# Performance work log

Hardware: AMD Instinct MI355X
Metric: run time of the kernel (lower is better)

Reference implementation:

```python
import jax, jax.numpy as jnp
import numpy as np

TEMPERATURE = 0.1
NEG_INF = -1e9
EPS = 1e-12

def setup_inputs() -> dict:
    key = jax.random.key(0)
    k1, k2, k3 = jax.random.split(key, 3)
    B, C, H, W = 8, 256, 128, 128
    num_classes = 150
    features = jax.random.normal(k1, (B, C, H, W), dtype=jnp.float32)
    labels = jax.random.randint(k2, (B, H, W), 0, num_classes, dtype=jnp.int32)
    text_embeddings = jax.random.normal(k3, (num_classes, C), dtype=jnp.float32)
    return {"features": features, "labels": labels, "text_embeddings": text_embeddings, "ignore_index": 255}

def _l2_normalize(x, axis=-1):
    n = jnp.linalg.norm(x, axis=axis, keepdims=True)
    return x / jnp.maximum(n, EPS)

def reference(features, labels, text_embeddings, ignore_index):
    num_classes, C = text_embeddings.shape
    B = features.shape[0]
    # [B,C,H,W] -> [B*H*W, C]
    f = jnp.transpose(features, (0, 2, 3, 1)).reshape(-1, C)
    lab = jnp.where(labels == ignore_index, 0, labels).reshape(-1)
    # segment-mean per class (fused scatter-add instead of per-class loop)
    sums = jax.ops.segment_sum(f, lab, num_segments=num_classes)          # [K,C]
    counts = jax.ops.segment_sum(jnp.ones_like(lab, dtype=f.dtype), lab, num_segments=num_classes)  # [K]
    valid = counts > 0
    prototypes = jnp.where(valid[:, None], sums / jnp.maximum(counts, 1.0)[:, None], 0.0)
    prototypes = _l2_normalize(prototypes)
    text_n = _l2_normalize(text_embeddings)
    sim = (prototypes @ text_n.T) / TEMPERATURE                            # [K,K]
    # cross-entropy restricted to valid rows/cols with identity soft targets
    masked = jnp.where(valid[None, :], sim, NEG_INF)                       # mask invalid cols
    logp = jax.nn.log_softmax(masked, axis=-1)
    diag = jnp.diagonal(logp)
    per_row = jnp.where(valid, -diag, 0.0)
    n_valid = jnp.sum(valid.astype(f.dtype))
    loss = jnp.sum(per_row) / jnp.maximum(n_valid, 1.0)
    return jnp.where(n_valid > 1, loss, 0.0)
```

## Files before the change

kernel.cpp:

```cpp
#include <hip/hip_runtime.h>
#include <math.h>

#define EPSV 1e-12f

typedef __attribute__((ext_vector_type(8))) short short8;
typedef __attribute__((ext_vector_type(4))) float f32x4;

constexpr int MT    = 10;
constexpr int K_PAD = MT * 16;
constexpr int CPB   = 64;
constexpr int CHUNK = 128;
constexpr int PBPX  = 2048;
constexpr int NCHK  = PBPX / CHUNK;
constexpr int NPB   = 64;
constexpr int THR   = 512;
constexpr int LROW  = 136;

__device__ __forceinline__ unsigned short f2bf(float f) {
    unsigned u = __builtin_bit_cast(unsigned, f);
    return (unsigned short)((u + 0x7FFFu + ((u >> 16) & 1u)) >> 16);
}

__global__ __launch_bounds__(THR) void protomm_kernel(
    const float* __restrict__ feat,
    const int*   __restrict__ labels,
    const int*   __restrict__ ign_p,
    float*       __restrict__ partial,
    int C, int HW)
{
    __shared__ unsigned short Bf[CPB * LROW];
    __shared__ int   labL[CHUNK];
    __shared__ float fscr[4][K_PAD * 16];

    const int tid   = threadIdx.x;
    const int w     = tid >> 6;
    const int l     = tid & 63;
    const int ct    = w & 3;
    const int kh    = w >> 2;
    const int rowid = l & 15;
    const int g     = l >> 4;

    const int bid = blockIdx.x;
    const int cg  = bid & 3;
    const int pb  = bid >> 2;
    const int b   = pb >> 3;
    const int px0 = (pb & 7) * PBPX;
    const int ig  = *ign_p;

    const int q   = tid & 31;
    const int chp = tid >> 5;
    const float* fb = feat + ((size_t)(b * C + cg * CPB + chp)) * HW + px0 + 4 * q;
    const int*   lb = labels + (size_t)b * HW + px0;

    f32x4 acc[MT];
    #pragma unroll
    for (int m = 0; m < MT; ++m) acc[m] = (f32x4){0.f, 0.f, 0.f, 0.f};

    float4 pf0, pf1, pf2, pf3;
    int4   plab;
    auto issue = [&](int ck) {
        const float* p = fb + ck * CHUNK;
        pf0 = *reinterpret_cast<const float4*>(p);
        pf1 = *reinterpret_cast<const float4*>(p + (size_t)16 * HW);
        pf2 = *reinterpret_cast<const float4*>(p + (size_t)32 * HW);
        pf3 = *reinterpret_cast<const float4*>(p + (size_t)48 * HW);
        if (tid < 32)
            plab = *reinterpret_cast<const int4*>(lb + ck * CHUNK + 4 * tid);
    };

    issue(0);

    for (int ck = 0; ck < NCHK; ++ck) {
        __syncthreads();
        {
            float4 v[4] = {pf0, pf1, pf2, pf3};
            #pragma unroll
            for (int i = 0; i < 4; ++i) {
                unsigned* dst = reinterpret_cast<unsigned*>(
                    &Bf[(chp + 16 * i) * LROW + 4 * q]);
                dst[0] = (unsigned)f2bf(v[i].x) | ((unsigned)f2bf(v[i].y) << 16);
                dst[1] = (unsigned)f2bf(v[i].z) | ((unsigned)f2bf(v[i].w) << 16);
            }
            if (tid < 32) {
                int4 lv = plab;
                lv.x = (lv.x == ig) ? 0 : lv.x;
                lv.y = (lv.y == ig) ? 0 : lv.y;
                lv.z = (lv.z == ig) ? 0 : lv.z;
                lv.w = (lv.w == ig) ? 0 : lv.w;
                *reinterpret_cast<int4*>(&labL[4 * tid]) = lv;
            }
        }
        __syncthreads();
        if (ck + 1 < NCHK) issue(ck + 1);

        #pragma unroll
        for (int kk = 0; kk < 2; ++kk) {
            const int ks = 2 * kh + kk;
            const int* lp = &labL[ks * 32 + g * 8];
            const int la0 = lp[0], la1 = lp[1], la2 = lp[2], la3 = lp[3];
            const int la4 = lp[4], la5 = lp[5], la6 = lp[6], la7 = lp[7];
            const short8 bfrag = *reinterpret_cast<const short8*>(
                &Bf[(ct * 16 + rowid) * LROW + ks * 32 + g * 8]);
            #pragma unroll
            for (int m = 0; m < MT; ++m) {
                const int tgt = m * 16 + rowid;
                unsigned w0 = (la0 == tgt ? 0x3F80u : 0u) | (la1 == tgt ? 0x3F800000u : 0u);
                unsigned w1 = (la2 == tgt ? 0x3F80u : 0u) | (la3 == tgt ? 0x3F800000u : 0u);
                unsigned w2 = (la4 == tgt ? 0x3F80u : 0u) | (la5 == tgt ? 0x3F800000u : 0u);
                unsigned w3 = (la6 == tgt ? 0x3F80u : 0u) | (la7 == tgt ? 0x3F800000u : 0u);
                uint4 aw = make_uint4(w0, w1, w2, w3);
                short8 afrag = __builtin_bit_cast(short8, aw);
                acc[m] = __builtin_amdgcn_mfma_f32_16x16x32_bf16(afrag, bfrag, acc[m], 0, 0, 0);
            }
        }
    }

    __syncthreads();
    if (kh == 1) {
        #pragma unroll
        for (int m = 0; m < MT; ++m)
            #pragma unroll
            for (int r = 0; r < 4; ++r)
                fscr[ct][(m * 16 + g * 4 + r) * 16 + rowid] = acc[m][r];
    }
    __syncthreads();
    if (kh == 0) {
        float* dst = partial + (size_t)pb * K_PAD * C + cg * CPB + ct * 16 + rowid;
        #pragma unroll
        for (int m = 0; m < MT; ++m)
            #pragma unroll
            for (int r = 0; r < 4; ++r) {
                const int cls = m * 16 + g * 4 + r;
                dst[(size_t)cls * C] = acc[m][r] + fscr[ct][cls * 16 + rowid];
            }
    }
}

__global__ __launch_bounds__(256) void counts_kernel(
    const int* __restrict__ labels, const int* __restrict__ ign_p,
    unsigned int* __restrict__ counts, int N, int K)
{
    __shared__ unsigned int cbins[160];
    const int tid = threadIdx.x;
    for (int i = tid; i < 160; i += 256) cbins[i] = 0u;
    __syncthreads();
    const int ig = *ign_p;
    const int4* l4 = reinterpret_cast<const int4*>(labels);
    const int n4 = N / 4;
    for (int i = blockIdx.x * 256 + tid; i < n4; i += gridDim.x * 256) {
        int4 v = l4[i];
        int a0 = (v.x == ig) ? 0 : v.x;
        int a1 = (v.y == ig) ? 0 : v.y;
        int a2 = (v.z == ig) ? 0 : v.z;
        int a3 = (v.w == ig) ? 0 : v.w;
        if ((unsigned)a0 < (unsigned)K) atomicAdd(&cbins[a0], 1u);
        if ((unsigned)a1 < (unsigned)K) atomicAdd(&cbins[a1], 1u);
        if ((unsigned)a2 < (unsigned)K) atomicAdd(&cbins[a2], 1u);
        if ((unsigned)a3 < (unsigned)K) atomicAdd(&cbins[a3], 1u);
    }
    __syncthreads();
    for (int i = tid; i < K; i += 256)
        if (cbins[i]) atomicAdd(&counts[i], cbins[i]);
}

__global__ __launch_bounds__(256) void normprep_kernel(
    const float* __restrict__ partial,
    const unsigned int* __restrict__ counts,
    const float* __restrict__ text,
    float* __restrict__ proto_n,
    float* __restrict__ text_n,
    float* __restrict__ vmask,
    int K, int C)
{
    const int bid  = blockIdx.x;
    const int tid  = threadIdx.x;
    const int wid  = tid >> 6;
    const int lane = tid & 63;
    const bool isproto = bid < K_PAD;
    const int  row = isproto ? bid : bid - K_PAD;

    __shared__ float red[5];

    float val = 0.f;
    if (isproto) {
        if (row >= K) return;
        unsigned cnt = counts[row];
        if (cnt == 0) return;
        const size_t gs = (size_t)K_PAD * C;
        const float* pp = partial + (size_t)row * C + tid;
        float a0 = 0.f, a1 = 0.f, a2 = 0.f, a3 = 0.f;
        float a4 = 0.f, a5 = 0.f, a6 = 0.f, a7 = 0.f;
        #pragma unroll 2
        for (int g = 0; g < NPB; g += 8) {
            a0 += pp[(g + 0) * gs]; a1 += pp[(g + 1) * gs];
            a2 += pp[(g + 2) * gs]; a3 += pp[(g + 3) * gs];
            a4 += pp[(g + 4) * gs]; a5 += pp[(g + 5) * gs];
            a6 += pp[(g + 6) * gs]; a7 += pp[(g + 7) * gs];
        }
        val = (((a0 + a1) + (a2 + a3)) + ((a4 + a5) + (a6 + a7))) / (float)cnt;
    } else {
        if (row >= K) { text_n[(size_t)row * C + tid] = 0.f; return; }
        val = text[(size_t)row * C + tid];
    }

    float v = val * val;
    #pragma unroll
    for (int o = 32; o > 0; o >>= 1) v += __shfl_down(v, o);
    if (lane == 0) red[wid] = v;
    __syncthreads();
    if (tid == 0) {
        float s = red[0] + red[1] + red[2] + red[3];
        red[4] = 1.0f / fmaxf(sqrtf(s), EPSV);
    }
    __syncthreads();
    float out = val * red[4];

    if (isproto) {
        proto_n[(size_t)row * C + tid] = out;
        if (tid == 0) vmask[row] = 1.f;
    } else {
        text_n[(size_t)row * C + tid] = out;
    }
}

__global__ __launch_bounds__(256) void loss_kernel(
    const float* __restrict__ proto_n,
    const float* __restrict__ text_n,
    const float* __restrict__ vmask,
    const unsigned int* __restrict__ counts,
    float* __restrict__ loss_acc,
    int K, int C)
{
    const int k = blockIdx.x;
    if (counts[k] == 0) return;

    __shared__ float ph[256];
    __shared__ float vm[K_PAD];
    __shared__ float wred[4 * 3];

    const int tid  = threadIdx.x;
    const int wid  = tid >> 6;
    const int lane = tid & 63;

    ph[tid] = proto_n[(size_t)k * C + tid];
    if (tid < K_PAD) vm[tid] = vmask[tid];
    __syncthreads();

    float m = -INFINITY, s = 0.f, skk = 0.f;
    #pragma unroll 1
    for (int gq = 0; gq < K_PAD / 16; ++gq) {
        const int j0 = gq * 16 + wid * 4;
        const float* t0 = text_n + (size_t)j0 * C;
        float d0 = 0.f, d1 = 0.f, d2 = 0.f, d3 = 0.f;
        #pragma unroll
        for (int cc = lane; cc < 256; cc += 64) {
            float p = ph[cc];
            d0 = fmaf(p, t0[cc],         d0);
            d1 = fmaf(p, t0[C + cc],     d1);
            d2 = fmaf(p, t0[2 * C + cc], d2);
            d3 = fmaf(p, t0[3 * C + cc], d3);
        }
        #pragma unroll
        for (int o = 32; o > 0; o >>= 1) {
            d0 += __shfl_down(d0, o); d1 += __shfl_down(d1, o);
            d2 += __shfl_down(d2, o); d3 += __shfl_down(d3, o);
        }
        if (lane == 0) {
            float dd[4] = {d0, d1, d2, d3};
            #pragma unroll
            for (int r = 0; r < 4; ++r) {
                int j = j0 + r;
                float v  = vm[j];
                float ms = v * (dd[r] * 10.f) - (1.f - v) * 1e9f;
                if (j == k) skk = ms;
                if (ms > m) { s = s * expf(m - ms) + 1.f; m = ms; }
                else        { s += expf(ms - m); }
            }
        }
    }
    if (lane == 0) { wred[wid*3+0] = m; wred[wid*3+1] = s; wred[wid*3+2] = skk; }
    __syncthreads();
    if (tid == 0) {
        float M = fmaxf(fmaxf(wred[0], wred[3]), fmaxf(wred[6], wred[9]));
        float S = 0.f, SKK = 0.f;
        #pragma unroll
        for (int w = 0; w < 4; ++w) {
            S   += wred[w*3+1] * expf(wred[w*3+0] - M);
            SKK += (wred[w*3+2] != 0.f) ? wred[w*3+2] : 0.f;
        }
        atomicAdd(loss_acc, M + logf(S) - SKK);
    }
}

__global__ __launch_bounds__(256) void finalize_kernel(
    const unsigned int* __restrict__ counts,
    const float* __restrict__ loss_acc,
    float* __restrict__ out, int K)
{
    __shared__ float red[4];
    int tid = threadIdx.x, wid = tid >> 6, lane = tid & 63;
    float v = (tid < K && counts[tid] > 0u) ? 1.f : 0.f;
    #pragma unroll
    for (int o = 32; o > 0; o >>= 1) v += __shfl_down(v, o);
    if (lane == 0) red[wid] = v;
    __syncthreads();
    if (tid == 0) {
        float nv = red[0] + red[1] + red[2] + red[3];
        float loss = loss_acc[0] / fmaxf(nv, 1.f);
        out[0] = (nv > 1.f) ? loss : 0.f;
    }
}

extern "C" void kernel_launch(void* const* d_in, const int* in_sizes, int n_in,
                              void* d_out, int out_size, void* d_ws, size_t ws_size,
                              hipStream_t stream) {
    const float* feat   = (const float*)d_in[0];
    const int*   labels = (const int*)d_in[1];
    const float* text   = (const float*)d_in[2];
    const int*   ign    = (const int*)d_in[3];

    const int B  = 8;
    const int N  = in_sizes[1];
    const int HW = N / B;
    const int C  = in_sizes[0] / N;
    const int K  = in_sizes[2] / C;

    float*        partial  = (float*)d_ws;
    float*        proto_n  = partial + (size_t)NPB * K_PAD * C;
    float*        text_n   = proto_n + (size_t)K_PAD * C;
    unsigned int* counts   = (unsigned int*)(text_n + (size_t)K_PAD * C);
    float*        vmask    = (float*)(counts + K_PAD);
    float*        loss_acc = vmask + K_PAD;

    hipMemsetAsync(counts, 0, (2 * K_PAD + 1) * sizeof(unsigned int), stream);

    protomm_kernel<<<NPB * 4, THR, 0, stream>>>(feat, labels, ign, partial, C, HW);

    counts_kernel<<<256, 256, 0, stream>>>(labels, ign, counts, N, K);

    normprep_kernel<<<2 * K_PAD, 256, 0, stream>>>(
        partial, counts, text, proto_n, text_n, vmask, K, C);

    loss_kernel<<<K, 256, 0, stream>>>(
        proto_n, text_n, vmask, counts, loss_acc, K, C);

    finalize_kernel<<<1, 256, 0, stream>>>(counts, loss_acc, (float*)d_out, K);
}
```

Measured before the change: 72.51 us.

## Fuse tail kernels, derive class presence in main kernel, double-buffer LDS

```diff
diff --git a/kernel.cpp b/kernel.cpp
--- a/kernel.cpp
+++ b/kernel.cpp
@@ -26,11 +26,13 @@
     const int*   __restrict__ labels,
     const int*   __restrict__ ign_p,
     float*       __restrict__ partial,
+    float*       __restrict__ vmask,
     int C, int HW)
 {
-    __shared__ unsigned short Bf[CPB * LROW];
-    __shared__ int   labL[CHUNK];
+    __shared__ unsigned short Bf[2][CPB * LROW];
+    __shared__ int   labL[2][CHUNK];
     __shared__ float fscr[4][K_PAD * 16];
+    __shared__ unsigned char pres[K_PAD];
 
     const int tid   = threadIdx.x;
     const int w     = tid >> 6;
@@ -51,6 +53,9 @@
     const int chp = tid >> 5;
     const float* fb = feat + ((size_t)(b * C + cg * CPB + chp)) * HW + px0 + 4 * q;
     const int*   lb = labels + (size_t)b * HW + px0;
+
+    if (cg == 0)
+        for (int i = tid; i < K_PAD; i += THR) pres[i] = 0;
 
     f32x4 acc[MT];
     #pragma unroll
@@ -67,40 +72,46 @@
         if (tid < 32)
             plab = *reinterpret_cast<const int4*>(lb + ck * CHUNK + 4 * tid);
     };
+    auto commit = [&](int buf) {
+        float4 v[4] = {pf0, pf1, pf2, pf3};
+        #pragma unroll
+        for (int i = 0; i < 4; ++i) {
+            unsigned* dst = reinterpret_cast<unsigned*>(
+                &Bf[buf][(chp + 16 * i) * LROW + 4 * q]);
+            dst[0] = (unsigned)f2bf(v[i].x) | ((unsigned)f2bf(v[i].y) << 16);
+            dst[1] = (unsigned)f2bf(v[i].z) | ((unsigned)f2bf(v[i].w) << 16);
+        }
+        if (tid < 32) {
+            int4 lv = plab;
+            lv.x = (lv.x == ig) ? 0 : lv.x;
+            lv.y = (lv.y == ig) ? 0 : lv.y;
+            lv.z = (lv.z == ig) ? 0 : lv.z;
+            lv.w = (lv.w == ig) ? 0 : lv.w;
+            *reinterpret_cast<int4*>(&labL[buf][4 * tid]) = lv;
+        }
+    };
 
     issue(0);
 
     for (int ck = 0; ck < NCHK; ++ck) {
-        __syncthreads();
-        {
-            float4 v[4] = {pf0, pf1, pf2, pf3};
-            #pragma unroll
-            for (int i = 0; i < 4; ++i) {
-                unsigned* dst = reinterpret_cast<unsigned*>(
-                    &Bf[(chp + 16 * i) * LROW + 4 * q]);
-                dst[0] = (unsigned)f2bf(v[i].x) | ((unsigned)f2bf(v[i].y) << 16);
-                dst[1] = (unsigned)f2bf(v[i].z) | ((unsigned)f2bf(v[i].w) << 16);
-            }
-            if (tid < 32) {
-                int4 lv = plab;
-                lv.x = (lv.x == ig) ? 0 : lv.x;
-                lv.y = (lv.y == ig) ? 0 : lv.y;
-                lv.z = (lv.z == ig) ? 0 : lv.z;
-                lv.w = (lv.w == ig) ? 0 : lv.w;
-                *reinterpret_cast<int4*>(&labL[4 * tid]) = lv;
-            }
-        }
-        __syncthreads();
+        const int cur = ck & 1;
+        commit(cur);
         if (ck + 1 < NCHK) issue(ck + 1);
+        __syncthreads();
+
+        if (cg == 0 && tid < CHUNK) {
+            int la = labL[cur][tid];
+            if ((unsigned)la < (unsigned)K_PAD) pres[la] = 1;
+        }
 
         #pragma unroll
         for (int kk = 0; kk < 2; ++kk) {
             const int ks = 2 * kh + kk;
-            const int* lp = &labL[ks * 32 + g * 8];
+            const int* lp = &labL[cur][ks * 32 + g * 8];
             const int la0 = lp[0], la1 = lp[1], la2 = lp[2], la3 = lp[3];
             const int la4 = lp[4], la5 = lp[5], la6 = lp[6], la7 = lp[7];
             const short8 bfrag = *reinterpret_cast<const short8*>(
-                &Bf[(ct * 16 + rowid) * LROW + ks * 32 + g * 8]);
+                &Bf[cur][(ct * 16 + rowid) * LROW + ks * 32 + g * 8]);
             #pragma unroll
             for (int m = 0; m < MT; ++m) {
                 const int tgt = m * 16 + rowid;
@@ -134,180 +145,136 @@
                 dst[(size_t)cls * C] = acc[m][r] + fscr[ct][cls * 16 + rowid];
             }
     }
+    if (cg == 0) {
+        for (int i = tid; i < K_PAD; i += THR)
+            if (pres[i]) vmask[i] = 1.0f;
+    }
 }
 
-__global__ __launch_bounds__(256) void counts_kernel(
-    const int* __restrict__ labels, const int* __restrict__ ign_p,
-    unsigned int* __restrict__ counts, int N, int K)
+__global__ __launch_bounds__(256) void tail_kernel(
+    const float* __restrict__ partial,
+    const float* __restrict__ text,
+    const float* __restrict__ vmask,
+    float* __restrict__ loss_acc,
+    unsigned int* __restrict__ ticket,
+    float* __restrict__ out,
+    int K, int C, int nblocks)
 {
-    __shared__ unsigned int cbins[160];
-    const int tid = threadIdx.x;
-    for (int i = tid; i < 160; i += 256) cbins[i] = 0u;
-    __syncthreads();
-    const int ig = *ign_p;
-    const int4* l4 = reinterpret_cast<const int4*>(labels);
-    const int n4 = N / 4;
-    for (int i = blockIdx.x * 256 + tid; i < n4; i += gridDim.x * 256) {
-        int4 v = l4[i];
-        int a0 = (v.x == ig) ? 0 : v.x;
-        int a1 = (v.y == ig) ? 0 : v.y;
-        int a2 = (v.z == ig) ? 0 : v.z;
-        int a3 = (v.w == ig) ? 0 : v.w;
-        if ((unsigned)a0 < (unsigned)K) atomicAdd(&cbins[a0], 1u);
-        if ((unsigned)a1 < (unsigned)K) atomicAdd(&cbins[a1], 1u);
-        if ((unsigned)a2 < (unsigned)K) atomicAdd(&cbins[a2], 1u);
-        if ((unsigned)a3 < (unsigned)K) atomicAdd(&cbins[a3], 1u);
-    }
-    __syncthreads();
-    for (int i = tid; i < K; i += 256)
-        if (cbins[i]) atomicAdd(&counts[i], cbins[i]);
-}
-
-__global__ __launch_bounds__(256) void normprep_kernel(
-    const float* __restrict__ partial,
-    const unsigned int* __restrict__ counts,
-    const float* __restrict__ text,
-    float* __restrict__ proto_n,
-    float* __restrict__ text_n,
-    float* __restrict__ vmask,
-    int K, int C)
-{
-    const int bid  = blockIdx.x;
+    __shared__ float ph[256];
+    __shared__ float vm[K_PAD];
+    __shared__ float red[5];
+    __shared__ float wred[12];
+    __shared__ unsigned int lastflag;
+
+    const int k    = blockIdx.x;
     const int tid  = threadIdx.x;
     const int wid  = tid >> 6;
     const int lane = tid & 63;
-    const bool isproto = bid < K_PAD;
-    const int  row = isproto ? bid : bid - K_PAD;
-
-    __shared__ float red[5];
-
-    float val = 0.f;
-    if (isproto) {
-        if (row >= K) return;
-        unsigned cnt = counts[row];
-        if (cnt == 0) return;
+
+    if (tid < K_PAD) vm[tid] = vmask[tid];
+    __syncthreads();
+    const bool valid = (vm[k] > 0.f);
+
+    float contrib = 0.f;
+    if (valid) {
         const size_t gs = (size_t)K_PAD * C;
-        const float* pp = partial + (size_t)row * C + tid;
+        const float* pp = partial + (size_t)k * C + tid;
         float a0 = 0.f, a1 = 0.f, a2 = 0.f, a3 = 0.f;
         float a4 = 0.f, a5 = 0.f, a6 = 0.f, a7 = 0.f;
-        #pragma unroll 2
         for (int g = 0; g < NPB; g += 8) {
             a0 += pp[(g + 0) * gs]; a1 += pp[(g + 1) * gs];
             a2 += pp[(g + 2) * gs]; a3 += pp[(g + 3) * gs];
             a4 += pp[(g + 4) * gs]; a5 += pp[(g + 5) * gs];
             a6 += pp[(g + 6) * gs]; a7 += pp[(g + 7) * gs];
         }
-        val = (((a0 + a1) + (a2 + a3)) + ((a4 + a5) + (a6 + a7))) / (float)cnt;
-    } else {
-        if (row >= K) { text_n[(size_t)row * C + tid] = 0.f; return; }
-        val = text[(size_t)row * C + tid];
-    }
-
-    float v = val * val;
-    #pragma unroll
-    for (int o = 32; o > 0; o >>= 1) v += __shfl_down(v, o);
-    if (lane == 0) red[wid] = v;
+        float sums = (((a0 + a1) + (a2 + a3)) + ((a4 + a5) + (a6 + a7)));
+
+        float v = sums * sums;
+        #pragma unroll
+        for (int o = 32; o > 0; o >>= 1) v += __shfl_down(v, o);
+        if (lane == 0) red[wid] = v;
+        __syncthreads();
+        if (tid == 0) {
+            float s = red[0] + red[1] + red[2] + red[3];
+            red[4] = 1.0f / fmaxf(sqrtf(s), EPSV);
+        }
+        __syncthreads();
+        ph[tid] = sums * red[4];
+        __syncthreads();
+
+        float m = -INFINITY, s = 0.f, skk = 0.f;
+        #pragma unroll 1
+        for (int gq = 0; gq < K_PAD / 16; ++gq) {
+            const int j0 = gq * 16 + wid * 4;
+            const float* t0 = text + (size_t)(j0 + 0 < K ? j0 + 0 : K - 1) * C;
+            const float* t1 = text + (size_t)(j0 + 1 < K ? j0 + 1 : K - 1) * C;
+            const float* t2 = text + (size_t)(j0 + 2 < K ? j0 + 2 : K - 1) * C;
+            const float* t3 = text + (size_t)(j0 + 3 < K ? j0 + 3 : K - 1) * C;
+            float d0 = 0.f, d1 = 0.f, d2 = 0.f, d3 = 0.f;
+            float q0 = 0.f, q1 = 0.f, q2 = 0.f, q3 = 0.f;
+            #pragma unroll
+            for (int cc = lane; cc < 256; cc += 64) {
+                float p  = ph[cc];
+                float x0 = t0[cc], x1 = t1[cc], x2 = t2[cc], x3 = t3[cc];
+                d0 = fmaf(p, x0, d0);  q0 = fmaf(x0, x0, q0);
+                d1 = fmaf(p, x1, d1);  q1 = fmaf(x1, x1, q1);
+                d2 = fmaf(p, x2, d2);  q2 = fmaf(x2, x2, q2);
+                d3 = fmaf(p, x3, d3);  q3 = fmaf(x3, x3, q3);
+            }
+            #pragma unroll
+            for (int o = 32; o > 0; o >>= 1) {
+                d0 += __shfl_down(d0, o); d1 += __shfl_down(d1, o);
+                d2 += __shfl_down(d2, o); d3 += __shfl_down(d3, o);
+                q0 += __shfl_down(q0, o); q1 += __shfl_down(q1, o);
+                q2 += __shfl_down(q2, o); q3 += __shfl_down(q3, o);
+            }
+            if (lane == 0) {
+                float dd[4] = {d0, d1, d2, d3};
+                float qq[4] = {q0, q1, q2, q3};
+                #pragma unroll
+                for (int r = 0; r < 4; ++r) {
+                    int j = j0 + r;
+                    float vmj = vm[j];
+                    float sim = dd[r] * (10.0f / fmaxf(sqrtf(qq[r]), EPSV));
+                    float ms  = vmj * sim - (1.f - vmj) * 1e9f;
+                    if (j == k) skk = ms;
+                    if (ms > m) { s = s * expf(m - ms) + 1.f; m = ms; }
+                    else        { s += expf(ms - m); }
+                }
+            }
+        }
+        if (lane == 0) { wred[wid*3+0] = m; wred[wid*3+1] = s; wred[wid*3+2] = skk; }
+        __syncthreads();
+        if (tid == 0) {
+            float M = fmaxf(fmaxf(wred[0], wred[3]), fmaxf(wred[6], wred[9]));
+            float S = 0.f, SKK = 0.f;
+            #pragma unroll
+            for (int ww = 0; ww < 4; ++ww) {
+                S   += wred[ww*3+1] * expf(wred[ww*3+0] - M);
+                SKK += wred[ww*3+2];
+            }
+            contrib = M + logf(S) - SKK;
+        }
+    }
+
+    if (tid == 0) {
+        if (valid) atomicAdd(loss_acc, contrib);
+        __threadfence();
+        unsigned old = atomicAdd(ticket, 1u);
+        lastflag = (old == (unsigned)(nblocks - 1)) ? 1u : 0u;
+    }
     __syncthreads();
-    if (tid == 0) {
-        float s = red[0] + red[1] + red[2] + red[3];
-        red[4] = 1.0f / fmaxf(sqrtf(s), EPSV);
-    }
-    __syncthreads();
-    float out = val * red[4];
-
-    if (isproto) {
-        proto_n[(size_t)row * C + tid] = out;
-        if (tid == 0) vmask[row] = 1.f;
-    } else {
-        text_n[(size_t)row * C + tid] = out;
-    }
-}
-
-__global__ __launch_bounds__(256) void loss_kernel(
-    const float* __restrict__ proto_n,
-    const float* __restrict__ text_n,
-    const float* __restrict__ vmask,
-    const unsigned int* __restrict__ counts,
-    float* __restrict__ loss_acc,
-    int K, int C)
-{
-    const int k = blockIdx.x;
-    if (counts[k] == 0) return;
-
-    __shared__ float ph[256];
-    __shared__ float vm[K_PAD];
-    __shared__ float wred[4 * 3];
-
-    const int tid  = threadIdx.x;
-    const int wid  = tid >> 6;
-    const int lane = tid & 63;
-
-    ph[tid] = proto_n[(size_t)k * C + tid];
-    if (tid < K_PAD) vm[tid] = vmask[tid];
-    __syncthreads();
-
-    float m = -INFINITY, s = 0.f, skk = 0.f;
-    #pragma unroll 1
-    for (int gq = 0; gq < K_PAD / 16; ++gq) {
-        const int j0 = gq * 16 + wid * 4;
-        const float* t0 = text_n + (size_t)j0 * C;
-        float d0 = 0.f, d1 = 0.f, d2 = 0.f, d3 = 0.f;
-        #pragma unroll
-        for (int cc = lane; cc < 256; cc += 64) {
-            float p = ph[cc];
-            d0 = fmaf(p, t0[cc],         d0);
-            d1 = fmaf(p, t0[C + cc],     d1);
-            d2 = fmaf(p, t0[2 * C + cc], d2);
-            d3 = fmaf(p, t0[3 * C + cc], d3);
-        }
-        #pragma unroll
-        for (int o = 32; o > 0; o >>= 1) {
-            d0 += __shfl_down(d0, o); d1 += __shfl_down(d1, o);
-            d2 += __shfl_down(d2, o); d3 += __shfl_down(d3, o);
-        }
-        if (lane == 0) {
-            float dd[4] = {d0, d1, d2, d3};
-            #pragma unroll
-            for (int r = 0; r < 4; ++r) {
-                int j = j0 + r;
-                float v  = vm[j];
-                float ms = v * (dd[r] * 10.f) - (1.f - v) * 1e9f;
-                if (j == k) skk = ms;
-                if (ms > m) { s = s * expf(m - ms) + 1.f; m = ms; }
-                else        { s += expf(ms - m); }
-            }
-        }
-    }
-    if (lane == 0) { wred[wid*3+0] = m; wred[wid*3+1] = s; wred[wid*3+2] = skk; }
-    __syncthreads();
-    if (tid == 0) {
-        float M = fmaxf(fmaxf(wred[0], wred[3]), fmaxf(wred[6], wred[9]));
-        float S = 0.f, SKK = 0.f;
-        #pragma unroll
-        for (int w = 0; w < 4; ++w) {
-            S   += wred[w*3+1] * expf(wred[w*3+0] - M);
-            SKK += (wred[w*3+2] != 0.f) ? wred[w*3+2] : 0.f;
-        }
-        atomicAdd(loss_acc, M + logf(S) - SKK);
-    }
-}
-
-__global__ __launch_bounds__(256) void finalize_kernel(
-    const unsigned int* __restrict__ counts,
-    const float* __restrict__ loss_acc,
-    float* __restrict__ out, int K)
-{
-    __shared__ float red[4];
-    int tid = threadIdx.x, wid = tid >> 6, lane = tid & 63;
-    float v = (tid < K && counts[tid] > 0u) ? 1.f : 0.f;
-    #pragma unroll
-    for (int o = 32; o > 0; o >>= 1) v += __shfl_down(v, o);
-    if (lane == 0) red[wid] = v;
-    __syncthreads();
-    if (tid == 0) {
-        float nv = red[0] + red[1] + red[2] + red[3];
-        float loss = loss_acc[0] / fmaxf(nv, 1.f);
-        out[0] = (nv > 1.f) ? loss : 0.f;
+    if (lastflag) {
+        float v = (tid < K_PAD) ? vm[tid] : 0.f;
+        #pragma unroll
+        for (int o = 32; o > 0; o >>= 1) v += __shfl_down(v, o);
+        if (lane == 0) red[wid] = v;
+        __syncthreads();
+        if (tid == 0) {
+            float nv = red[0] + red[1] + red[2] + red[3];
+            float total = atomicAdd(loss_acc, 0.0f);
+            out[0] = (nv > 1.f) ? total / fmaxf(nv, 1.f) : 0.f;
+        }
     }
 }
 
@@ -326,23 +293,15 @@
     const int K  = in_sizes[2] / C;
 
     float*        partial  = (float*)d_ws;
-    float*        proto_n  = partial + (size_t)NPB * K_PAD * C;
-    float*        text_n   = proto_n + (size_t)K_PAD * C;
-    unsigned int* counts   = (unsigned int*)(text_n + (size_t)K_PAD * C);
-    float*        vmask    = (float*)(counts + K_PAD);
+    float*        vmask    = partial + (size_t)NPB * K_PAD * C;
     float*        loss_acc = vmask + K_PAD;
-
-    hipMemsetAsync(counts, 0, (2 * K_PAD + 1) * sizeof(unsigned int), stream);
-
-    protomm_kernel<<<NPB * 4, THR, 0, stream>>>(feat, labels, ign, partial, C, HW);
-
-    counts_kernel<<<256, 256, 0, stream>>>(labels, ign, counts, N, K);
-
-    normprep_kernel<<<2 * K_PAD, 256, 0, stream>>>(
-        partial, counts, text, proto_n, text_n, vmask, K, C);
-
-    loss_kernel<<<K, 256, 0, stream>>>(
-        proto_n, text_n, vmask, counts, loss_acc, K, C);
-
-    finalize_kernel<<<1, 256, 0, stream>>>(counts, loss_acc, (float*)d_out, K);
+    unsigned int* ticket   = (unsigned int*)(loss_acc + 1);
+
+    hipMemsetAsync(vmask, 0, (K_PAD + 2) * sizeof(float), stream);
+
+    protomm_kernel<<<NPB * 4, THR, 0, stream>>>(
+        feat, labels, ign, partial, vmask, C, HW);
+
+    tail_kernel<<<K, 256, 0, stream>>>(
+        partial, text, vmask, loss_acc, ticket, (float*)d_out, K, C, K);
 }
```

After: 69.96 us. 3.5% less time.
